# Optimization experiments

Measured on AMD Instinct MI355X. Metric: run time of the kernel, lower is better.

The kernel has to match this reference:

```python
import jax, jax.numpy as jnp
import numpy as np

N_NODES = 40000
N_EDGES = 640000
D = 128  # in_channels == out_channels (required by the module's math)


def setup_inputs() -> dict:
    key = jax.random.key(0)
    ks = jax.random.split(key, 8)
    s = 1.0 / np.sqrt(D)  # torch Linear default init scale
    x = jax.random.normal(ks[0], (N_NODES, D), dtype=jnp.float32)
    edge_index = jax.random.randint(ks[1], (2, N_EDGES), 0, N_NODES, dtype=jnp.int64)
    Wn_w = jax.random.uniform(ks[2], (D, D), jnp.float32, -s, s)
    Wn_b = jax.random.uniform(ks[3], (D,), jnp.float32, -s, s)
    Wg_w = jax.random.uniform(ks[4], (D, D), jnp.float32, -s, s)
    Wg_b = jax.random.uniform(ks[5], (D,), jnp.float32, -s, s)
    Wa_w = jax.random.uniform(ks[6], (D, D), jnp.float32, -s, s)
    Wa_b = jax.random.uniform(ks[7], (D,), jnp.float32, -s, s)
    return {"x": x, "edge_index": edge_index,
            "Wn_w": Wn_w, "Wn_b": Wn_b,
            "Wg_w": Wg_w, "Wg_b": Wg_b,
            "Wa_w": Wa_w, "Wa_b": Wa_b}


def reference(x, edge_index, Wn_w, Wn_b, Wg_w, Wg_b, Wa_w, Wa_b):
    row, col = edge_index[0], edge_index[1]
    x_col = x[col]                                  # [E, D] gather
    alpha = jax.nn.sigmoid(x_col @ Wa_w + Wa_b)     # [E, D] edge attention
    neigh = x_col * alpha                           # [E, D]
    aggr = jax.ops.segment_sum(neigh, row, num_segments=x.shape[0])  # [N, D]
    out = jnp.tanh((x @ Wn_w + Wn_b) + (aggr @ Wg_w + Wg_b))
    return out  # dropout p=0.0 is identity
```

## Files before the change

### kernel.cpp

```cpp
#include <hip/hip_runtime.h>

#define NN 40000
#define NE 640000
#define D 128
#define CAP 64

typedef __attribute__((ext_vector_type(8))) short short8;
typedef __attribute__((ext_vector_type(4))) float f32x4;
typedef __attribute__((ext_vector_type(4))) int i32x4;

__device__ __forceinline__ short f2b(float v) {
  unsigned int u = __builtin_bit_cast(unsigned int, v);
  u = (u + 0x7fffu + ((u >> 16) & 1u)) >> 16;
  return (short)u;
}
__device__ __forceinline__ float b2f(short s) {
  unsigned int u = ((unsigned int)(unsigned short)s) << 16;
  return __builtin_bit_cast(float, u);
}

__global__ __launch_bounds__(256) void k_prep(
    const float* __restrict__ Wn, const float* __restrict__ Wg,
    const float* __restrict__ Wa, short* __restrict__ WnT,
    short* __restrict__ WgThi, short* __restrict__ WgTlo,
    short* __restrict__ WaT, int* __restrict__ cnt) {
  int i = blockIdx.x * 256 + threadIdx.x;
  int k = i >> 7, c = i & 127;
  WnT[c * D + k] = f2b(Wn[k * D + c]);
  WaT[c * D + k] = f2b(Wa[k * D + c]);
  float v = Wg[k * D + c];
  short hi = f2b(v);
  WgThi[c * D + k] = hi;
  WgTlo[c * D + k] = f2b(v - b2f(hi));
  if (i < 10000) {
    i32x4 z = {0, 0, 0, 0};
    *(i32x4*)(cnt + i * 4) = z;
  }
}

__global__ __launch_bounds__(256) void k_node(
    const float* __restrict__ x, const short* __restrict__ WaT,
    const short* __restrict__ WnT, const float* __restrict__ ba,
    float* __restrict__ xn_out, short* __restrict__ h_out) {
  int r0 = blockIdx.x * 16;
  int w = threadIdx.x >> 6, l = threadIdx.x & 63;
  int g = l >> 4, c16 = l & 15;
  int rowA = r0 + c16;

  short8 a[4];
#pragma unroll
  for (int kt = 0; kt < 4; ++kt) {
    const float* p = x + (size_t)rowA * D + kt * 32 + g * 8;
    f32x4 v0 = *(const f32x4*)p;
    f32x4 v1 = *(const f32x4*)(p + 4);
    short8 t;
    t[0] = f2b(v0[0]); t[1] = f2b(v0[1]); t[2] = f2b(v0[2]); t[3] = f2b(v0[3]);
    t[4] = f2b(v1[0]); t[5] = f2b(v1[1]); t[6] = f2b(v1[2]); t[7] = f2b(v1[3]);
    a[kt] = t;
  }

#pragma unroll
  for (int u = 0; u < 2; ++u) {
    int ct = w * 2 + u;
    int cc = ct * 16 + c16;
    f32x4 c = {0.f, 0.f, 0.f, 0.f};
#pragma unroll
    for (int kt = 0; kt < 4; ++kt) {
      short8 b = *(const short8*)(WaT + (size_t)cc * D + kt * 32 + g * 8);
      c = __builtin_amdgcn_mfma_f32_16x16x32_bf16(a[kt], b, c, 0, 0, 0);
    }
    float bav = ba[cc];
#pragma unroll
    for (int r = 0; r < 4; ++r) {
      int rr = r0 + g * 4 + r;
      float t = c[r] + bav;
      float al = 1.0f / (1.0f + __expf(-t));
      float xv = x[(size_t)rr * D + cc];
      h_out[(size_t)rr * D + cc] = f2b(xv * al);
    }
    f32x4 cn = {0.f, 0.f, 0.f, 0.f};
#pragma unroll
    for (int kt = 0; kt < 4; ++kt) {
      short8 b = *(const short8*)(WnT + (size_t)cc * D + kt * 32 + g * 8);
      cn = __builtin_amdgcn_mfma_f32_16x16x32_bf16(a[kt], b, cn, 0, 0, 0);
    }
#pragma unroll
    for (int r = 0; r < 4; ++r) {
      int rr = r0 + g * 4 + r;
      xn_out[(size_t)rr * D + cc] = cn[r];
    }
  }
}

__global__ __launch_bounds__(256) void k_fill(
    const int* __restrict__ ei, int* __restrict__ cnt,
    int* __restrict__ bucket) {
  int e = blockIdx.x * 256 + threadIdx.x;
  if (e >= NE) return;
  int r = ei[e];
  int c = ei[NE + e];
  int slot = atomicAdd(&cnt[r], 1);
  if (slot < CAP) bucket[r * CAP + slot] = c;
}

__global__ __launch_bounds__(256) void k_aggr(
    const int* __restrict__ cnt, const int* __restrict__ bucket,
    const short* __restrict__ h, float* __restrict__ s) {
  int l = threadIdx.x & 63;
  int n = blockIdx.x * 4 + (threadIdx.x >> 6);
  if (n >= NN) return;
  int g = l >> 4, i = l & 15;
  int deg = cnt[n];
  deg = deg < CAP ? deg : CAP;
  int bc = bucket[n * CAP + l];
  float acc[8];
#pragma unroll
  for (int q = 0; q < 8; ++q) acc[q] = 0.f;

  int j = 0;
  for (; j + 8 <= deg; j += 8) {
    int c0 = __shfl(bc, j + g);
    int c1 = __shfl(bc, j + 4 + g);
    short8 v0 = *(const short8*)(h + (size_t)c0 * D + i * 8);
    short8 v1 = *(const short8*)(h + (size_t)c1 * D + i * 8);
#pragma unroll
    for (int q = 0; q < 8; ++q) acc[q] += b2f(v0[q]);
#pragma unroll
    for (int q = 0; q < 8; ++q) acc[q] += b2f(v1[q]);
  }
  for (; j < deg; j += 4) {
    int src = j + g;
    int clamped = src < deg ? src : deg - 1;
    int c0 = __shfl(bc, clamped);
    if (src < deg) {
      short8 v0 = *(const short8*)(h + (size_t)c0 * D + i * 8);
#pragma unroll
      for (int q = 0; q < 8; ++q) acc[q] += b2f(v0[q]);
    }
  }

#pragma unroll
  for (int q = 0; q < 8; ++q) {
    acc[q] += __shfl_xor(acc[q], 16);
    acc[q] += __shfl_xor(acc[q], 32);
  }
  if (g == 0) {
    f32x4 lo = {acc[0], acc[1], acc[2], acc[3]};
    f32x4 hi = {acc[4], acc[5], acc[6], acc[7]};
    *(f32x4*)(s + (size_t)n * D + i * 8) = lo;
    *(f32x4*)(s + (size_t)n * D + i * 8 + 4) = hi;
  }
}

__global__ __launch_bounds__(256) void k_final(
    const float* __restrict__ s, const short* __restrict__ WgThi,
    const short* __restrict__ WgTlo, const float* __restrict__ bn,
    const float* __restrict__ bg, float* __restrict__ out) {
  int r0 = blockIdx.x * 16;
  int w = threadIdx.x >> 6, l = threadIdx.x & 63;
  int g = l >> 4, c16 = l & 15;
  int rowA = r0 + c16;

  short8 ahi[4], alo[4];
#pragma unroll
  for (int kt = 0; kt < 4; ++kt) {
    const float* p = s + (size_t)rowA * D + kt * 32 + g * 8;
    f32x4 v0 = *(const f32x4*)p;
    f32x4 v1 = *(const f32x4*)(p + 4);
    short8 hi, lo;
#pragma unroll
    for (int jq = 0; jq < 4; ++jq) {
      short hh = f2b(v0[jq]);
      hi[jq] = hh;
      lo[jq] = f2b(v0[jq] - b2f(hh));
    }
#pragma unroll
    for (int jq = 0; jq < 4; ++jq) {
      short hh = f2b(v1[jq]);
      hi[4 + jq] = hh;
      lo[4 + jq] = f2b(v1[jq] - b2f(hh));
    }
    ahi[kt] = hi;
    alo[kt] = lo;
  }

#pragma unroll
  for (int u = 0; u < 2; ++u) {
    int ct = w * 2 + u;
    int cc = ct * 16 + c16;
    f32x4 c = {0.f, 0.f, 0.f, 0.f};
#pragma unroll
    for (int kt = 0; kt < 4; ++kt) {
      short8 bh = *(const short8*)(WgThi + (size_t)cc * D + kt * 32 + g * 8);
      short8 bl = *(const short8*)(WgTlo + (size_t)cc * D + kt * 32 + g * 8);
      c = __builtin_amdgcn_mfma_f32_16x16x32_bf16(ahi[kt], bh, c, 0, 0, 0);
      c = __builtin_amdgcn_mfma_f32_16x16x32_bf16(alo[kt], bh, c, 0, 0, 0);
      c = __builtin_amdgcn_mfma_f32_16x16x32_bf16(ahi[kt], bl, c, 0, 0, 0);
    }
    float bias = bn[cc] + bg[cc];
#pragma unroll
    for (int r = 0; r < 4; ++r) {
      int rr = r0 + g * 4 + r;
      float z = c[r] + out[(size_t)rr * D + cc] + bias;
      out[(size_t)rr * D + cc] = tanhf(z);
    }
  }
}

extern "C" void kernel_launch(void* const* d_in, const int* in_sizes, int n_in,
                              void* d_out, int out_size, void* d_ws,
                              size_t ws_size, hipStream_t stream) {
  const float* x = (const float*)d_in[0];
  const int* ei = (const int*)d_in[1];
  const float* Wn_w = (const float*)d_in[2];
  const float* Wn_b = (const float*)d_in[3];
  const float* Wg_w = (const float*)d_in[4];
  const float* Wg_b = (const float*)d_in[5];
  const float* Wa_w = (const float*)d_in[6];
  const float* Wa_b = (const float*)d_in[7];

  char* ws = (char*)d_ws;
  short* WaT = (short*)(ws + 0);
  short* WnT = (short*)(ws + 32 * 1024);
  short* WgThi = (short*)(ws + 64 * 1024);
  short* WgTlo = (short*)(ws + 96 * 1024);
  int* cnt = (int*)(ws + 128 * 1024);
  float* s = (float*)(ws + 512 * 1024);
  short* h = (short*)(ws + 512 * 1024 + (size_t)NN * D * 4);
  int* bucket = (int*)(ws + 512 * 1024 + (size_t)NN * D * 6);
  float* out = (float*)d_out;

  k_prep<<<64, 256, 0, stream>>>(Wn_w, Wg_w, Wa_w, WnT, WgThi, WgTlo, WaT, cnt);
  k_node<<<NN / 16, 256, 0, stream>>>(x, WaT, WnT, Wa_b, out, h);
  k_fill<<<(NE + 255) / 256, 256, 0, stream>>>(ei, cnt, bucket);
  k_aggr<<<NN / 4, 256, 0, stream>>>(cnt, bucket, h, s);
  k_final<<<NN / 16, 256, 0, stream>>>(s, WgThi, WgTlo, Wn_b, Wg_b, out);
}
```

Before: 126.4 us.

## Fuse edge bucketing into node kernel and aggregation into final GEMM

Merges the edge-bucket fill into the node attention kernel by giving extra blocks to the edge work, and fuses neighbor aggregation with the final projection through shared memory, dropping the fp32 aggregate buffer round-trip. The x@Wn GEMM moves into the final kernel, reading a stored bf16 copy of x instead of writing and re-reading an fp32 partial output. This cuts two launches and removes several large global reads and writes. In exchange the final kernel has fewer, heavier blocks, whose gather latency now sits in front of the MFMA work.

```diff
diff --git a/kernel.cpp b/kernel.cpp
--- a/kernel.cpp
+++ b/kernel.cpp
@@ -38,11 +38,21 @@
   }
 }
 
-__global__ __launch_bounds__(256) void k_node(
+__global__ __launch_bounds__(256) void k_nf(
     const float* __restrict__ x, const short* __restrict__ WaT,
-    const short* __restrict__ WnT, const float* __restrict__ ba,
-    float* __restrict__ xn_out, short* __restrict__ h_out) {
-  int r0 = blockIdx.x * 16;
+    const float* __restrict__ ba, short* __restrict__ h_out,
+    short* __restrict__ xbf_out, const int* __restrict__ ei,
+    int* __restrict__ cnt, int* __restrict__ bucket) {
+  int bid = blockIdx.x;
+  if (bid >= 2500) {
+    int e = (bid - 2500) * 256 + threadIdx.x;
+    int r = ei[e];
+    int c = ei[NE + e];
+    int slot = atomicAdd(&cnt[r], 1);
+    if (slot < CAP) bucket[r * CAP + slot] = c;
+    return;
+  }
+  int r0 = bid * 16;
   int w = threadIdx.x >> 6, l = threadIdx.x & 63;
   int g = l >> 4, c16 = l & 15;
   int rowA = r0 + c16;
@@ -57,6 +67,7 @@
     t[0] = f2b(v0[0]); t[1] = f2b(v0[1]); t[2] = f2b(v0[2]); t[3] = f2b(v0[3]);
     t[4] = f2b(v1[0]); t[5] = f2b(v1[1]); t[6] = f2b(v1[2]); t[7] = f2b(v1[3]);
     a[kt] = t;
+    *(short8*)(xbf_out + (size_t)rowA * D + kt * 32 + g * 8) = t;
   }
 
 #pragma unroll
@@ -78,93 +89,71 @@
       float xv = x[(size_t)rr * D + cc];
       h_out[(size_t)rr * D + cc] = f2b(xv * al);
     }
-    f32x4 cn = {0.f, 0.f, 0.f, 0.f};
-#pragma unroll
-    for (int kt = 0; kt < 4; ++kt) {
-      short8 b = *(const short8*)(WnT + (size_t)cc * D + kt * 32 + g * 8);
-      cn = __builtin_amdgcn_mfma_f32_16x16x32_bf16(a[kt], b, cn, 0, 0, 0);
-    }
-#pragma unroll
-    for (int r = 0; r < 4; ++r) {
-      int rr = r0 + g * 4 + r;
-      xn_out[(size_t)rr * D + cc] = cn[r];
-    }
-  }
-}
-
-__global__ __launch_bounds__(256) void k_fill(
-    const int* __restrict__ ei, int* __restrict__ cnt,
-    int* __restrict__ bucket) {
-  int e = blockIdx.x * 256 + threadIdx.x;
-  if (e >= NE) return;
-  int r = ei[e];
-  int c = ei[NE + e];
-  int slot = atomicAdd(&cnt[r], 1);
-  if (slot < CAP) bucket[r * CAP + slot] = c;
-}
-
-__global__ __launch_bounds__(256) void k_aggr(
+  }
+}
+
+__global__ __launch_bounds__(256) void k_fused(
     const int* __restrict__ cnt, const int* __restrict__ bucket,
-    const short* __restrict__ h, float* __restrict__ s) {
-  int l = threadIdx.x & 63;
-  int n = blockIdx.x * 4 + (threadIdx.x >> 6);
-  if (n >= NN) return;
-  int g = l >> 4, i = l & 15;
-  int deg = cnt[n];
-  deg = deg < CAP ? deg : CAP;
-  int bc = bucket[n * CAP + l];
-  float acc[8];
-#pragma unroll
-  for (int q = 0; q < 8; ++q) acc[q] = 0.f;
-
-  int j = 0;
-  for (; j + 8 <= deg; j += 8) {
-    int c0 = __shfl(bc, j + g);
-    int c1 = __shfl(bc, j + 4 + g);
-    short8 v0 = *(const short8*)(h + (size_t)c0 * D + i * 8);
-    short8 v1 = *(const short8*)(h + (size_t)c1 * D + i * 8);
-#pragma unroll
-    for (int q = 0; q < 8; ++q) acc[q] += b2f(v0[q]);
-#pragma unroll
-    for (int q = 0; q < 8; ++q) acc[q] += b2f(v1[q]);
-  }
-  for (; j < deg; j += 4) {
-    int src = j + g;
-    int clamped = src < deg ? src : deg - 1;
-    int c0 = __shfl(bc, clamped);
-    if (src < deg) {
-      short8 v0 = *(const short8*)(h + (size_t)c0 * D + i * 8);
-#pragma unroll
-      for (int q = 0; q < 8; ++q) acc[q] += b2f(v0[q]);
-    }
-  }
-
-#pragma unroll
-  for (int q = 0; q < 8; ++q) {
-    acc[q] += __shfl_xor(acc[q], 16);
-    acc[q] += __shfl_xor(acc[q], 32);
-  }
-  if (g == 0) {
-    f32x4 lo = {acc[0], acc[1], acc[2], acc[3]};
-    f32x4 hi = {acc[4], acc[5], acc[6], acc[7]};
-    *(f32x4*)(s + (size_t)n * D + i * 8) = lo;
-    *(f32x4*)(s + (size_t)n * D + i * 8 + 4) = hi;
-  }
-}
-
-__global__ __launch_bounds__(256) void k_final(
-    const float* __restrict__ s, const short* __restrict__ WgThi,
+    const short* __restrict__ h, const short* __restrict__ xbf,
+    const short* __restrict__ WnT, const short* __restrict__ WgThi,
     const short* __restrict__ WgTlo, const float* __restrict__ bn,
     const float* __restrict__ bg, float* __restrict__ out) {
-  int r0 = blockIdx.x * 16;
+  __shared__ float st[16][132];
   int w = threadIdx.x >> 6, l = threadIdx.x & 63;
-  int g = l >> 4, c16 = l & 15;
-  int rowA = r0 + c16;
-
-  short8 ahi[4], alo[4];
+  int g = l >> 4, i = l & 15;
+  int base = blockIdx.x * 16;
+
+#pragma unroll
+  for (int v = 0; v < 4; ++v) {
+    int n = base + w * 4 + v;
+    int deg = cnt[n];
+    deg = deg < CAP ? deg : CAP;
+    int bc = bucket[(size_t)n * CAP + l];
+    float acc[8];
+#pragma unroll
+    for (int q = 0; q < 8; ++q) acc[q] = 0.f;
+
+    int j = 0;
+    for (; j + 8 <= deg; j += 8) {
+      int c0 = __shfl(bc, j + g);
+      int c1 = __shfl(bc, j + 4 + g);
+      short8 v0 = *(const short8*)(h + (size_t)c0 * D + i * 8);
+      short8 v1 = *(const short8*)(h + (size_t)c1 * D + i * 8);
+#pragma unroll
+      for (int q = 0; q < 8; ++q) acc[q] += b2f(v0[q]);
+#pragma unroll
+      for (int q = 0; q < 8; ++q) acc[q] += b2f(v1[q]);
+    }
+    for (; j < deg; j += 4) {
+      int src = j + g;
+      int clamped = src < deg ? src : deg - 1;
+      int c0 = __shfl(bc, clamped);
+      if (src < deg) {
+        short8 v0 = *(const short8*)(h + (size_t)c0 * D + i * 8);
+#pragma unroll
+        for (int q = 0; q < 8; ++q) acc[q] += b2f(v0[q]);
+      }
+    }
+#pragma unroll
+    for (int q = 0; q < 8; ++q) {
+      acc[q] += __shfl_xor(acc[q], 16);
+      acc[q] += __shfl_xor(acc[q], 32);
+    }
+    if (g == 0) {
+      f32x4 lo = {acc[0], acc[1], acc[2], acc[3]};
+      f32x4 hi = {acc[4], acc[5], acc[6], acc[7]};
+      *(f32x4*)&st[w * 4 + v][i * 8] = lo;
+      *(f32x4*)&st[w * 4 + v][i * 8 + 4] = hi;
+    }
+  }
+  __syncthreads();
+
+  short8 axf[4], ash[4], asl[4];
+  int rowG = base + i;
 #pragma unroll
   for (int kt = 0; kt < 4; ++kt) {
-    const float* p = s + (size_t)rowA * D + kt * 32 + g * 8;
+    axf[kt] = *(const short8*)(xbf + (size_t)rowG * D + kt * 32 + g * 8);
+    const float* p = &st[i][kt * 32 + g * 8];
     f32x4 v0 = *(const f32x4*)p;
     f32x4 v1 = *(const f32x4*)(p + 4);
     short8 hi, lo;
@@ -180,29 +169,33 @@
       hi[4 + jq] = hh;
       lo[4 + jq] = f2b(v1[jq] - b2f(hh));
     }
-    ahi[kt] = hi;
-    alo[kt] = lo;
+    ash[kt] = hi;
+    asl[kt] = lo;
   }
 
 #pragma unroll
   for (int u = 0; u < 2; ++u) {
     int ct = w * 2 + u;
-    int cc = ct * 16 + c16;
+    int cc = ct * 16 + i;
     f32x4 c = {0.f, 0.f, 0.f, 0.f};
+#pragma unroll
+    for (int kt = 0; kt < 4; ++kt) {
+      short8 b = *(const short8*)(WnT + (size_t)cc * D + kt * 32 + g * 8);
+      c = __builtin_amdgcn_mfma_f32_16x16x32_bf16(axf[kt], b, c, 0, 0, 0);
+    }
 #pragma unroll
     for (int kt = 0; kt < 4; ++kt) {
       short8 bh = *(const short8*)(WgThi + (size_t)cc * D + kt * 32 + g * 8);
       short8 bl = *(const short8*)(WgTlo + (size_t)cc * D + kt * 32 + g * 8);
-      c = __builtin_amdgcn_mfma_f32_16x16x32_bf16(ahi[kt], bh, c, 0, 0, 0);
-      c = __builtin_amdgcn_mfma_f32_16x16x32_bf16(alo[kt], bh, c, 0, 0, 0);
-      c = __builtin_amdgcn_mfma_f32_16x16x32_bf16(ahi[kt], bl, c, 0, 0, 0);
+      c = __builtin_amdgcn_mfma_f32_16x16x32_bf16(ash[kt], bh, c, 0, 0, 0);
+      c = __builtin_amdgcn_mfma_f32_16x16x32_bf16(asl[kt], bh, c, 0, 0, 0);
+      c = __builtin_amdgcn_mfma_f32_16x16x32_bf16(ash[kt], bl, c, 0, 0, 0);
     }
     float bias = bn[cc] + bg[cc];
 #pragma unroll
     for (int r = 0; r < 4; ++r) {
-      int rr = r0 + g * 4 + r;
-      float z = c[r] + out[(size_t)rr * D + cc] + bias;
-      out[(size_t)rr * D + cc] = tanhf(z);
+      int rr = base + g * 4 + r;
+      out[(size_t)rr * D + cc] = tanhf(c[r] + bias);
     }
   }
 }
@@ -225,14 +218,13 @@
   short* WgThi = (short*)(ws + 64 * 1024);
   short* WgTlo = (short*)(ws + 96 * 1024);
   int* cnt = (int*)(ws + 128 * 1024);
-  float* s = (float*)(ws + 512 * 1024);
-  short* h = (short*)(ws + 512 * 1024 + (size_t)NN * D * 4);
-  int* bucket = (int*)(ws + 512 * 1024 + (size_t)NN * D * 6);
+  short* h = (short*)(ws + 512 * 1024);
+  short* xbf = (short*)(ws + 512 * 1024 + (size_t)NN * D * 2);
+  int* bucket = (int*)(ws + 512 * 1024 + (size_t)NN * D * 4);
   float* out = (float*)d_out;
 
   k_prep<<<64, 256, 0, stream>>>(Wn_w, Wg_w, Wa_w, WnT, WgThi, WgTlo, WaT, cnt);
-  k_node<<<NN / 16, 256, 0, stream>>>(x, WaT, WnT, Wa_b, out, h);
-  k_fill<<<(NE + 255) / 256, 256, 0, stream>>>(ei, cnt, bucket);
-  k_aggr<<<NN / 4, 256, 0, stream>>>(cnt, bucket, h, s);
-  k_final<<<NN / 16, 256, 0, stream>>>(s, WgThi, WgTlo, Wn_b, Wg_b, out);
-}
+  k_nf<<<5000, 256, 0, stream>>>(x, WaT, Wa_b, h, xbf, ei, cnt, bucket);
+  k_fused<<<2500, 256, 0, stream>>>(cnt, bucket, h, xbf, WnT, WgThi, WgTlo,
+                                    Wn_b, Wg_b, out);
+}
```

Result: slower. 134.6 us (+6.5%).
